# Kernel tuning notes

Measured on AMD Instinct MI355X. Metric: run time of the kernel, lower is better.

Reference implementation:

```python
import jax, jax.numpy as jnp
import numpy as np

N = 20000
E = N * 16
K = 6  # DynamicEdgeConv default k


def feast_conv(x, edge_index, W, u, c, b):
    # PyG FeaStConv with aggr='mean' and added self-loops.
    # q_h = softmax_h(u_h . (x_j - x_i) + c_h); msg = sum_h q_h * (W_h x_j)
    n = x.shape[0]
    heads = u.shape[1]
    out_ch = W.shape[1] // heads
    loops = jnp.arange(n)
    src = jnp.concatenate([edge_index[0], loops])  # x_j (source)
    dst = jnp.concatenate([edge_index[1], loops])  # x_i (target)
    xi = x[dst]
    xj = x[src]
    q = jax.nn.softmax((xj - xi) @ u + c, axis=-1)           # [E+N, H]
    m = (xj @ W).reshape(-1, heads, out_ch)                   # [E+N, H, O]
    msg = (m * q[..., None]).sum(axis=1)                      # [E+N, O]
    agg = jax.ops.segment_sum(msg, dst, num_segments=n)
    cnt = jax.ops.segment_sum(jnp.ones((dst.shape[0],), x.dtype), dst, num_segments=n)
    return agg / jnp.maximum(cnt, 1.0)[:, None] + b


def dynamic_edge_conv(x, W1, b1, W2, b2, k=K):
    # knn_graph (Euclidean, no self-loops) + EdgeConv with max aggregation.
    n = x.shape[0]
    sq = jnp.sum(x * x, axis=1)
    d = sq[:, None] + sq[None, :] - 2.0 * (x @ x.T)           # [N, N] squared dists
    d = d.at[jnp.arange(n), jnp.arange(n)].set(jnp.inf)       # loop=False
    idx = jax.lax.stop_gradient(jax.lax.top_k(-d, k)[1])      # [N, k] neighbors of i
    xj = x[idx]                                               # [N, k, C]
    xi = x[:, None, :]
    tmp = jnp.concatenate([jnp.broadcast_to(xi, xj.shape), xj - xi], axis=-1)
    h = jax.nn.relu(tmp @ W1 + b1) @ W2 + b2                  # mlp on each edge
    return h.max(axis=1)                                      # scatter-max == max over fixed k


def forward(x, edge_index, params):
    (cW1, cu1, cc1, cb1, cW3, cu3, cc3, cb3,
     e1W1, e1b1, e1W2, e1b2, e2W1, e2b1, e2W2, e2b2,
     l1W, l1b, l2W, l2b, l3W, l3b, oW, ob) = params
    x1 = jax.nn.relu(feast_conv(x, edge_index, cW1, cu1, cc1, cb1))      # [N,16]
    y1 = jax.nn.relu(dynamic_edge_conv(x1, e1W1, e1b1, e1W2, e1b2))      # [N,32]
    cat0 = jnp.concatenate([x1, y1], axis=1)                              # [N,48]
    # conv2 output is dead code in the original forward (overwritten), skipped
    y2 = jax.nn.relu(dynamic_edge_conv(y1, e2W1, e2b1, e2W2, e2b2))      # [N,32]
    x3 = jax.nn.relu(feast_conv(cat0, edge_index, cW3, cu3, cc3, cb3))   # [N,64]
    cat1 = jnp.concatenate([x3, y2], axis=1)                              # [N,96]
    h = jax.nn.relu(cat1 @ l1W + l1b)
    h = jax.nn.relu(h @ l2W + l2b)
    h = jax.nn.relu(h @ l3W + l3b)  # double relu in source is idempotent
    return jax.nn.sigmoid(h @ oW + ob)                                    # [N,1]


def setup_inputs() -> dict:
    key = jax.random.key(0)
    ks = jax.random.split(key, 20)
    rn = lambda k, s: jax.random.normal(k, s, jnp.float32) * 0.1
    z = lambda s: jnp.zeros(s, jnp.float32)
    return {
        "x": jax.random.normal(ks[0], (N, 16), jnp.float32),
        "edge_index": jax.random.randint(ks[1], (2, E), 0, N, dtype=jnp.int32),
        # conv1: FeaStConv(16 -> 16, heads=1)
        "cW1": rn(ks[2], (16, 16)), "cu1": rn(ks[3], (16, 1)), "cc1": z((1,)), "cb1": z((16,)),
        # conv3: FeaStConv(48 -> 64, heads=1)
        "cW3": rn(ks[4], (48, 64)), "cu3": rn(ks[5], (48, 1)), "cc3": z((1,)), "cb3": z((64,)),
        # edge1 mlp: Linear(2*16, 32), Linear(32, 32)
        "e1W1": rn(ks[6], (32, 32)), "e1b1": z((32,)), "e1W2": rn(ks[7], (32, 32)), "e1b2": z((32,)),
        # edge2 mlp: Linear(2*32, 32), Linear(32, 32)
        "e2W1": rn(ks[8], (64, 32)), "e2b1": z((32,)), "e2W2": rn(ks[9], (32, 32)), "e2b2": z((32,)),
        # dense head
        "l1W": rn(ks[10], (96, 96)), "l1b": z((96,)),
        "l2W": rn(ks[11], (96, 32)), "l2b": z((32,)),
        "l3W": rn(ks[12], (32, 8)), "l3b": z((8,)),
        "oW": rn(ks[13], (8, 1)), "ob": z((1,)),
    }


def reference(x, edge_index, cW1, cu1, cc1, cb1, cW3, cu3, cc3, cb3,
              e1W1, e1b1, e1W2, e1b2, e2W1, e2b1, e2W2, e2b2,
              l1W, l1b, l2W, l2b, l3W, l3b, oW, ob):
    params = (cW1, cu1, cc1, cb1, cW3, cu3, cc3, cb3,
              e1W1, e1b1, e1W2, e1b2, e2W1, e2b1, e2W2, e2b2,
              l1W, l1b, l2W, l2b, l3W, l3b, oW, ob)
    return forward(x, edge_index, params)
```

## Files before the change

### kernel.cpp

```cpp
#include <hip/hip_runtime.h>
#include <cstdint>

constexpr int Nn = 20000;
constexpr int Ee = 320000;
constexpr int KN = 6;

__global__ __launch_bounds__(256) void scatter16(const float* __restrict__ x,
                                                 const int* __restrict__ ei,
                                                 float* __restrict__ agg,
                                                 int* __restrict__ cnt) {
  int tid = blockIdx.x * 256 + threadIdx.x;
  int e = tid >> 4, c = tid & 15;
  if (e >= Ee) return;
  int s = ei[e], d = ei[Ee + e];
  unsafeAtomicAdd(&agg[d * 16 + c], x[s * 16 + c]);
  if (c == 0) atomicAdd(&cnt[d], 1);
}

__global__ __launch_bounds__(256) void feast1_fin(const float* __restrict__ x,
                                                  const float* __restrict__ agg,
                                                  const int* __restrict__ cnt,
                                                  const float* __restrict__ W,
                                                  const float* __restrict__ b,
                                                  float* __restrict__ x1,
                                                  float* __restrict__ sq) {
  __shared__ float sW[256];
  __shared__ float sb[16];
  sW[threadIdx.x] = W[threadIdx.x];
  if (threadIdx.x < 16) sb[threadIdx.x] = b[threadIdx.x];
  __syncthreads();
  int n = blockIdx.x * 256 + threadIdx.x;
  if (n >= Nn) return;
  float inv = 1.0f / (float)(cnt[n] + 1);
  float v[16];
#pragma unroll
  for (int c = 0; c < 16; ++c) v[c] = (agg[n * 16 + c] + x[n * 16 + c]) * inv;
  float s = 0.0f;
#pragma unroll
  for (int o = 0; o < 16; ++o) {
    float a = sb[o];
#pragma unroll
    for (int c = 0; c < 16; ++c) a = fmaf(v[c], sW[c * 16 + o], a);
    a = fmaxf(a, 0.0f);
    x1[n * 16 + o] = a;
    s = fmaf(a, a, s);
  }
  sq[n] = s;
}

__device__ __forceinline__ void bsins6(float d, int j, float (&bd)[KN], int (&bi)[KN]) {
#pragma unroll
  for (int k = KN - 1; k >= 1; --k) {
    const bool up = d < bd[k - 1];
    const bool at = d < bd[k];
    bd[k] = up ? bd[k - 1] : (at ? d : bd[k]);
    bi[k] = up ? bi[k - 1] : (at ? j : bi[k]);
  }
  const bool at0 = d < bd[0];
  bd[0] = at0 ? d : bd[0];
  bi[0] = at0 ? j : bi[0];
}

template <int C, int U, int TPB>
__global__ __launch_bounds__(TPB, 4) void knn_part(const float* __restrict__ xf,
                                                   const float* __restrict__ sq,
                                                   float* __restrict__ pd,
                                                   int* __restrict__ pi, int chunk) {
  const int row = blockIdx.x * TPB + (int)threadIdx.x;
  const int p = blockIdx.y;
  const int j0 = p * chunk;
  int j1 = j0 + chunk;
  if (j1 > Nn) j1 = Nn;

  float xi[C];
  {
    const float* src = xf + (size_t)(row < Nn ? row : 0) * C;
#pragma unroll
    for (int c = 0; c < C; ++c) xi[c] = src[c];
  }
  float bd[KN];
  int bi[KN];
#pragma unroll
  for (int k = 0; k < KN; ++k) { bd[k] = __builtin_inff(); bi[k] = -1; }

  for (int j = j0; j < j1; j += U) {
    float sv[U];
#pragma unroll
    for (int u = 0; u < U; ++u) {
      const float* xjp = xf + (size_t)(j + u) * C;
      float sqj = sq[j + u];
      float acc = 0.0f;
#pragma unroll
      for (int c = 0; c < C; ++c) acc = fmaf(xi[c], xjp[c], acc);
      float d = fmaf(-2.0f, acc, sqj);
      sv[u] = (j + u == row) ? __builtin_inff() : d;
    }
#pragma unroll
    for (int u = 0; u < U; ++u) bsins6(sv[u], j + u, bd, bi);
  }

  if (row < Nn) {
    size_t base = ((size_t)p * Nn + row) * KN;
    for (int k = 0; k < KN; ++k) { pd[base + k] = bd[k]; pi[base + k] = bi[k]; }
  }
}

__global__ __launch_bounds__(256) void knn_merge(const float* __restrict__ pd,
                                                 const int* __restrict__ pi,
                                                 int* __restrict__ idx, int P) {
  int row = blockIdx.x * 256 + threadIdx.x;
  if (row >= Nn) return;
  float bd[KN];
  int bi[KN];
#pragma unroll
  for (int k = 0; k < KN; ++k) { bd[k] = __builtin_inff(); bi[k] = -1; }
  for (int p = 0; p < P; ++p) {
    size_t base = ((size_t)p * Nn + row) * KN;
#pragma unroll
    for (int k = 0; k < KN; ++k) {
      float d = pd[base + k];
      int id = pi[base + k];
      bsins6(d, id, bd, bi);
    }
  }
  for (int k = 0; k < KN; ++k) idx[row * KN + k] = bi[k];
}

__global__ __launch_bounds__(256) void edge_mlp1(const float* __restrict__ xin,
                                                 const int* __restrict__ idx,
                                                 const float* __restrict__ W1,
                                                 const float* __restrict__ b1,
                                                 const float* __restrict__ W2,
                                                 const float* __restrict__ b2,
                                                 float* __restrict__ yout,
                                                 float* __restrict__ sqout) {
  __shared__ float sW1[1024], sW2[1024], sb1[32], sb2[32];
  __shared__ float xv[8][16], tmp[8][32], hv[8][32];
  int t = threadIdx.x & 31, g = threadIdx.x >> 5;
  for (int i = threadIdx.x; i < 1024; i += 256) { sW1[i] = W1[i]; sW2[i] = W2[i]; }
  if (threadIdx.x < 32) { sb1[threadIdx.x] = b1[threadIdx.x]; sb2[threadIdx.x] = b2[threadIdx.x]; }
  int node = blockIdx.x * 8 + g;
  bool valid = node < Nn;
  int nn = valid ? node : 0;
  if (t < 16) { float v = xin[nn * 16 + t]; xv[g][t] = v; tmp[g][t] = v; }
  __syncthreads();
  float acc = -__builtin_inff();
  for (int k = 0; k < KN; ++k) {
    int j = idx[nn * KN + k];
    if (t < 16) tmp[g][16 + t] = xin[j * 16 + t] - xv[g][t];
    __syncthreads();
    float h = sb1[t];
#pragma unroll
    for (int c = 0; c < 32; ++c) h = fmaf(tmp[g][c], sW1[c * 32 + t], h);
    h = fmaxf(h, 0.0f);
    hv[g][t] = h;
    __syncthreads();
    float o = sb2[t];
#pragma unroll
    for (int c = 0; c < 32; ++c) o = fmaf(hv[g][c], sW2[c * 32 + t], o);
    acc = fmaxf(acc, o);
  }
  float yv = fmaxf(acc, 0.0f);
  if (valid) yout[node * 32 + t] = yv;
  float s = yv * yv;
  s += __shfl_xor(s, 16, 32);
  s += __shfl_xor(s, 8, 32);
  s += __shfl_xor(s, 4, 32);
  s += __shfl_xor(s, 2, 32);
  s += __shfl_xor(s, 1, 32);
  if (valid && t == 0) sqout[node] = s;
}

__global__ __launch_bounds__(256) void edge_mlp2(const float* __restrict__ yin,
                                                 const int* __restrict__ idx,
                                                 const float* __restrict__ W1,
                                                 const float* __restrict__ b1,
                                                 const float* __restrict__ W2,
                                                 const float* __restrict__ b2,
                                                 float* __restrict__ yout) {
  __shared__ float sW1[2048], sW2[1024], sb1[32], sb2[32];
  __shared__ float xv[8][32], tmp[8][64], hv[8][32];
  int t = threadIdx.x & 31, g = threadIdx.x >> 5;
  for (int i = threadIdx.x; i < 2048; i += 256) sW1[i] = W1[i];
  for (int i = threadIdx.x; i < 1024; i += 256) sW2[i] = W2[i];
  if (threadIdx.x < 32) { sb1[threadIdx.x] = b1[threadIdx.x]; sb2[threadIdx.x] = b2[threadIdx.x]; }
  int node = blockIdx.x * 8 + g;
  bool valid = node < Nn;
  int nn = valid ? node : 0;
  { float v = yin[nn * 32 + t]; xv[g][t] = v; tmp[g][t] = v; }
  __syncthreads();
  float acc = -__builtin_inff();
  for (int k = 0; k < KN; ++k) {
    int j = idx[nn * KN + k];
    tmp[g][32 + t] = yin[j * 32 + t] - xv[g][t];
    __syncthreads();
    float h = sb1[t];
#pragma unroll
    for (int c = 0; c < 64; ++c) h = fmaf(tmp[g][c], sW1[c * 32 + t], h);
    h = fmaxf(h, 0.0f);
    hv[g][t] = h;
    __syncthreads();
    float o = sb2[t];
#pragma unroll
    for (int c = 0; c < 32; ++c) o = fmaf(hv[g][c], sW2[c * 32 + t], o);
    acc = fmaxf(acc, o);
  }
  if (valid) yout[node * 32 + t] = fmaxf(acc, 0.0f);
}

__global__ __launch_bounds__(256) void scatter48(const float* __restrict__ x1,
                                                 const float* __restrict__ y1,
                                                 const int* __restrict__ ei,
                                                 float* __restrict__ agg) {
  int tid = blockIdx.x * 256 + threadIdx.x;
  int e = tid / 48, c = tid - e * 48;
  if (e >= Ee) return;
  int s = ei[e], d = ei[Ee + e];
  float v = (c < 16) ? x1[s * 16 + c] : y1[s * 32 + (c - 16)];
  unsafeAtomicAdd(&agg[d * 48 + c], v);
}

__global__ __launch_bounds__(256) void feast3_fin(const float* __restrict__ x1,
                                                  const float* __restrict__ y1,
                                                  const float* __restrict__ agg,
                                                  const int* __restrict__ cnt,
                                                  const float* __restrict__ W,
                                                  const float* __restrict__ b,
                                                  float* __restrict__ x3) {
  __shared__ float sW[3072];
  __shared__ float sb[64];
  for (int i = threadIdx.x; i < 3072; i += 256) sW[i] = W[i];
  if (threadIdx.x < 64) sb[threadIdx.x] = b[threadIdx.x];
  __syncthreads();
  int n = blockIdx.x * 256 + threadIdx.x;
  if (n >= Nn) return;
  float inv = 1.0f / (float)(cnt[n] + 1);
  float v[48];
#pragma unroll
  for (int c = 0; c < 16; ++c) v[c] = (agg[n * 48 + c] + x1[n * 16 + c]) * inv;
#pragma unroll
  for (int c = 16; c < 48; ++c) v[c] = (agg[n * 48 + c] + y1[n * 32 + (c - 16)]) * inv;
  for (int o = 0; o < 64; ++o) {
    float a = sb[o];
#pragma unroll
    for (int c = 0; c < 48; ++c) a = fmaf(v[c], sW[c * 64 + o], a);
    x3[n * 64 + o] = fmaxf(a, 0.0f);
  }
}

__global__ __launch_bounds__(256) void final_mlp(const float* __restrict__ x3,
                                                 const float* __restrict__ y2,
                                                 const float* __restrict__ l1W,
                                                 const float* __restrict__ l1b,
                                                 const float* __restrict__ l2W,
                                                 const float* __restrict__ l2b,
                                                 const float* __restrict__ l3W,
                                                 const float* __restrict__ l3b,
                                                 const float* __restrict__ oW,
                                                 const float* __restrict__ ob,
                                                 float* __restrict__ out) {
  __shared__ float cat[2][96], h1[2][96], h2[2][32], h3[2][8];
  int g = threadIdx.x >> 7, t = threadIdx.x & 127;
  int node = blockIdx.x * 2 + g;
  bool valid = node < Nn;
  int nn = valid ? node : 0;
  if (t < 96) cat[g][t] = (t < 64) ? x3[nn * 64 + t] : y2[nn * 32 + (t - 64)];
  __syncthreads();
  if (t < 96) {
    float a = l1b[t];
#pragma unroll
    for (int c = 0; c < 96; ++c) a = fmaf(cat[g][c], l1W[c * 96 + t], a);
    h1[g][t] = fmaxf(a, 0.0f);
  }
  __syncthreads();
  if (t < 32) {
    float a = l2b[t];
#pragma unroll
    for (int c = 0; c < 96; ++c) a = fmaf(h1[g][c], l2W[c * 32 + t], a);
    h2[g][t] = fmaxf(a, 0.0f);
  }
  __syncthreads();
  if (t < 8) {
    float a = l3b[t];
#pragma unroll
    for (int c = 0; c < 32; ++c) a = fmaf(h2[g][c], l3W[c * 8 + t], a);
    h3[g][t] = fmaxf(a, 0.0f);
  }
  __syncthreads();
  if (t == 0 && valid) {
    float a = ob[0];
#pragma unroll
    for (int c = 0; c < 8; ++c) a = fmaf(h3[g][c], oW[c], a);
    out[node] = 1.0f / (1.0f + expf(-a));
  }
}

extern "C" void kernel_launch(void* const* d_in, const int* in_sizes, int n_in,
                              void* d_out, int out_size, void* d_ws, size_t ws_size,
                              hipStream_t stream) {
  const float* x = (const float*)d_in[0];
  const int* ei = (const int*)d_in[1];
  const float* cW1 = (const float*)d_in[2];
  const float* cb1 = (const float*)d_in[5];
  const float* cW3 = (const float*)d_in[6];
  const float* cb3 = (const float*)d_in[9];
  const float* e1W1 = (const float*)d_in[10];
  const float* e1b1 = (const float*)d_in[11];
  const float* e1W2 = (const float*)d_in[12];
  const float* e1b2 = (const float*)d_in[13];
  const float* e2W1 = (const float*)d_in[14];
  const float* e2b1 = (const float*)d_in[15];
  const float* e2W2 = (const float*)d_in[16];
  const float* e2b2 = (const float*)d_in[17];
  const float* l1W = (const float*)d_in[18];
  const float* l1b = (const float*)d_in[19];
  const float* l2W = (const float*)d_in[20];
  const float* l2b = (const float*)d_in[21];
  const float* l3W = (const float*)d_in[22];
  const float* l3b = (const float*)d_in[23];
  const float* oW = (const float*)d_in[24];
  const float* ob = (const float*)d_in[25];
  float* out = (float*)d_out;

  char* p = (char*)d_ws;
  auto alloc = [&](size_t bytes) {
    char* r = p;
    p += (bytes + 255) & ~(size_t)255;
    return r;
  };
  float* x1 = (float*)alloc((size_t)Nn * 16 * 4);
  float* y1 = (float*)alloc((size_t)Nn * 32 * 4);
  float* y2 = (float*)alloc((size_t)Nn * 32 * 4);
  float* x3 = (float*)alloc((size_t)Nn * 64 * 4);
  float* agg = (float*)alloc((size_t)Nn * 48 * 4);
  int* cnt = (int*)alloc((size_t)Nn * 4);
  float* sqb = (float*)alloc((size_t)Nn * 4);
  int* idx1 = (int*)alloc((size_t)Nn * KN * 4);
  int* idx2 = (int*)alloc((size_t)Nn * KN * 4);
  size_t fixed_bytes = (size_t)(p - (char*)d_ws);
  size_t per_chunk = (size_t)Nn * KN * 4 * 2 + 512;
  int P = 16;
  if (fixed_bytes + (size_t)P * per_chunk > ws_size) {
    size_t avail = ws_size > fixed_bytes ? ws_size - fixed_bytes : 0;
    int pmax = (int)(avail / per_chunk);
    P = pmax < 1 ? 1 : pmax;
    if (P > 16) P = 16;
  }
  float* pd = (float*)alloc((size_t)P * Nn * KN * 4);
  int* pi = (int*)alloc((size_t)P * Nn * KN * 4);
  int chunk = (((Nn + P - 1) / P) + 3) & ~3;

  hipMemsetAsync(agg, 0, (size_t)Nn * 16 * 4, stream);
  hipMemsetAsync(cnt, 0, (size_t)Nn * 4, stream);
  scatter16<<<(Ee * 16) / 256, 256, 0, stream>>>(x, ei, agg, cnt);
  feast1_fin<<<(Nn + 255) / 256, 256, 0, stream>>>(x, agg, cnt, cW1, cb1, x1, sqb);

  {
    dim3 grid((Nn + 255) / 256, P);
    knn_part<16, 4, 256><<<grid, 256, 0, stream>>>(x1, sqb, pd, pi, chunk);
    knn_merge<<<(Nn + 255) / 256, 256, 0, stream>>>(pd, pi, idx1, P);
  }

  edge_mlp1<<<(Nn + 7) / 8, 256, 0, stream>>>(x1, idx1, e1W1, e1b1, e1W2, e1b2, y1, sqb);

  {
    dim3 grid((Nn + 255) / 256, P);
    knn_part<32, 2, 256><<<grid, 256, 0, stream>>>(y1, sqb, pd, pi, chunk);
    knn_merge<<<(Nn + 255) / 256, 256, 0, stream>>>(pd, pi, idx2, P);
  }

  edge_mlp2<<<(Nn + 7) / 8, 256, 0, stream>>>(y1, idx2, e2W1, e2b1, e2W2, e2b2, y2);

  hipMemsetAsync(agg, 0, (size_t)Nn * 48 * 4, stream);
  scatter48<<<(Ee * 48) / 256, 256, 0, stream>>>(x1, y1, ei, agg);
  feast3_fin<<<(Nn + 255) / 256, 256, 0, stream>>>(x1, y1, agg, cnt, cW3, cb3, x3);

  final_mlp<<<(Nn + 1) / 2, 256, 0, stream>>>(x3, y2, l1W, l1b, l2W, l2b, l3W, l3b,
                                              oW, ob, out);
}
```

Baseline: 1.685 ms.

## Split kNN into value-only pass, threshold, and filtered index pass

The kNN search now makes two passes. The first keeps only the 6 smallest distances per row, using a cheap min/max network with no index tracking, and a merge kernel turns these into a per-row 6th-nearest threshold. A second pass recomputes all distances and runs the full index-tracking insertion only for candidates at or below that threshold, so most insertion work is skipped. The cost is computing the full distance matrix twice and launching two extra kernels, and the launch-bounds occupancy hint is dropped.

```diff
diff --git a/kernel.cpp b/kernel.cpp
--- a/kernel.cpp
+++ b/kernel.cpp
@@ -48,6 +48,12 @@
   sq[n] = s;
 }
 
+__device__ __forceinline__ void bsv6(float d, float (&bd)[KN]) {
+#pragma unroll
+  for (int k = KN - 1; k >= 1; --k) bd[k] = fminf(fmaxf(bd[k - 1], d), bd[k]);
+  bd[0] = fminf(bd[0], d);
+}
+
 __device__ __forceinline__ void bsins6(float d, int j, float (&bd)[KN], int (&bi)[KN]) {
 #pragma unroll
   for (int k = KN - 1; k >= 1; --k) {
@@ -62,10 +68,9 @@
 }
 
 template <int C, int U, int TPB>
-__global__ __launch_bounds__(TPB, 4) void knn_part(const float* __restrict__ xf,
-                                                   const float* __restrict__ sq,
-                                                   float* __restrict__ pd,
-                                                   int* __restrict__ pi, int chunk) {
+__global__ __launch_bounds__(TPB) void knn_val(const float* __restrict__ xf,
+                                               const float* __restrict__ sq,
+                                               float* __restrict__ pv, int chunk) {
   const int row = blockIdx.x * TPB + (int)threadIdx.x;
   const int p = blockIdx.y;
   const int j0 = p * chunk;
@@ -79,12 +84,10 @@
     for (int c = 0; c < C; ++c) xi[c] = src[c];
   }
   float bd[KN];
-  int bi[KN];
-#pragma unroll
-  for (int k = 0; k < KN; ++k) { bd[k] = __builtin_inff(); bi[k] = -1; }
+#pragma unroll
+  for (int k = 0; k < KN; ++k) bd[k] = __builtin_inff();
 
   for (int j = j0; j < j1; j += U) {
-    float sv[U];
 #pragma unroll
     for (int u = 0; u < U; ++u) {
       const float* xjp = xf + (size_t)(j + u) * C;
@@ -93,10 +96,78 @@
 #pragma unroll
       for (int c = 0; c < C; ++c) acc = fmaf(xi[c], xjp[c], acc);
       float d = fmaf(-2.0f, acc, sqj);
+      d = (j + u == row) ? __builtin_inff() : d;
+      bsv6(d, bd);
+    }
+  }
+
+  if (row < Nn) {
+    size_t base = ((size_t)p * Nn + row) * KN;
+#pragma unroll
+    for (int k = 0; k < KN; ++k) pv[base + k] = bd[k];
+  }
+}
+
+__global__ __launch_bounds__(256) void knn_thr(const float* __restrict__ pv,
+                                               float* __restrict__ thr, int P) {
+  int row = blockIdx.x * 256 + threadIdx.x;
+  if (row >= Nn) return;
+  float bd[KN];
+#pragma unroll
+  for (int k = 0; k < KN; ++k) bd[k] = __builtin_inff();
+  for (int p = 0; p < P; ++p) {
+    size_t base = ((size_t)p * Nn + row) * KN;
+#pragma unroll
+    for (int k = 0; k < KN; ++k) bsv6(pv[base + k], bd);
+  }
+  thr[row] = bd[5];
+}
+
+template <int C, int U, int TPB>
+__global__ __launch_bounds__(TPB) void knn_hit(const float* __restrict__ xf,
+                                               const float* __restrict__ sq,
+                                               const float* __restrict__ thr,
+                                               float* __restrict__ pd,
+                                               int* __restrict__ pi, int chunk) {
+  const int row = blockIdx.x * TPB + (int)threadIdx.x;
+  const int p = blockIdx.y;
+  const int j0 = p * chunk;
+  int j1 = j0 + chunk;
+  if (j1 > Nn) j1 = Nn;
+
+  const int rc = row < Nn ? row : 0;
+  float xi[C];
+  {
+    const float* src = xf + (size_t)rc * C;
+#pragma unroll
+    for (int c = 0; c < C; ++c) xi[c] = src[c];
+  }
+  const float thrv = thr[rc];
+  float bd[KN];
+  int bi[KN];
+#pragma unroll
+  for (int k = 0; k < KN; ++k) { bd[k] = __builtin_inff(); bi[k] = -1; }
+
+  for (int j = j0; j < j1; j += U) {
+    float sv[U];
+#pragma unroll
+    for (int u = 0; u < U; ++u) {
+      const float* xjp = xf + (size_t)(j + u) * C;
+      float sqj = sq[j + u];
+      float acc = 0.0f;
+#pragma unroll
+      for (int c = 0; c < C; ++c) acc = fmaf(xi[c], xjp[c], acc);
+      float d = fmaf(-2.0f, acc, sqj);
       sv[u] = (j + u == row) ? __builtin_inff() : d;
     }
-#pragma unroll
-    for (int u = 0; u < U; ++u) bsins6(sv[u], j + u, bd, bi);
+    float mn = sv[0];
+#pragma unroll
+    for (int u = 1; u < U; ++u) mn = fminf(mn, sv[u]);
+    if (mn <= thrv) {
+#pragma unroll
+      for (int u = 0; u < U; ++u)
+        if (sv[u] <= thrv) bsins6(sv[u], j + u, bd, bi);
+    }
   }
 
   if (row < Nn) {
@@ -118,9 +189,7 @@
     size_t base = ((size_t)p * Nn + row) * KN;
 #pragma unroll
     for (int k = 0; k < KN; ++k) {
-      float d = pd[base + k];
-      int id = pi[base + k];
-      bsins6(d, id, bd, bi);
+      bsins6(pd[base + k], pi[base + k], bd, bi);
     }
   }
   for (int k = 0; k < KN; ++k) idx[row * KN + k] = bi[k];
@@ -335,6 +404,7 @@
   float* agg = (float*)alloc((size_t)Nn * 48 * 4);
   int* cnt = (int*)alloc((size_t)Nn * 4);
   float* sqb = (float*)alloc((size_t)Nn * 4);
+  float* thr = (float*)alloc((size_t)Nn * 4);
   int* idx1 = (int*)alloc((size_t)Nn * KN * 4);
   int* idx2 = (int*)alloc((size_t)Nn * KN * 4);
   size_t fixed_bytes = (size_t)(p - (char*)d_ws);
@@ -349,31 +419,36 @@
   float* pd = (float*)alloc((size_t)P * Nn * KN * 4);
   int* pi = (int*)alloc((size_t)P * Nn * KN * 4);
   int chunk = (((Nn + P - 1) / P) + 3) & ~3;
+  const int gx = (Nn + 255) / 256;
 
   hipMemsetAsync(agg, 0, (size_t)Nn * 16 * 4, stream);
   hipMemsetAsync(cnt, 0, (size_t)Nn * 4, stream);
   scatter16<<<(Ee * 16) / 256, 256, 0, stream>>>(x, ei, agg, cnt);
-  feast1_fin<<<(Nn + 255) / 256, 256, 0, stream>>>(x, agg, cnt, cW1, cb1, x1, sqb);
+  feast1_fin<<<gx, 256, 0, stream>>>(x, agg, cnt, cW1, cb1, x1, sqb);
 
   {
-    dim3 grid((Nn + 255) / 256, P);
-    knn_part<16, 4, 256><<<grid, 256, 0, stream>>>(x1, sqb, pd, pi, chunk);
-    knn_merge<<<(Nn + 255) / 256, 256, 0, stream>>>(pd, pi, idx1, P);
+    dim3 grid(gx, P);
+    knn_val<16, 4, 256><<<grid, 256, 0, stream>>>(x1, sqb, pd, chunk);
+    knn_thr<<<gx, 256, 0, stream>>>(pd, thr, P);
+    knn_hit<16, 4, 256><<<grid, 256, 0, stream>>>(x1, sqb, thr, pd, pi, chunk);
+    knn_merge<<<gx, 256, 0, stream>>>(pd, pi, idx1, P);
   }
 
   edge_mlp1<<<(Nn + 7) / 8, 256, 0, stream>>>(x1, idx1, e1W1, e1b1, e1W2, e1b2, y1, sqb);
 
   {
-    dim3 grid((Nn + 255) / 256, P);
-    knn_part<32, 2, 256><<<grid, 256, 0, stream>>>(y1, sqb, pd, pi, chunk);
-    knn_merge<<<(Nn + 255) / 256, 256, 0, stream>>>(pd, pi, idx2, P);
+    dim3 grid(gx, P);
+    knn_val<32, 2, 256><<<grid, 256, 0, stream>>>(y1, sqb, pd, chunk);
+    knn_thr<<<gx, 256, 0, stream>>>(pd, thr, P);
+    knn_hit<32, 2, 256><<<grid, 256, 0, stream>>>(y1, sqb, thr, pd, pi, chunk);
+    knn_merge<<<gx, 256, 0, stream>>>(pd, pi, idx2, P);
   }
 
   edge_mlp2<<<(Nn + 7) / 8, 256, 0, stream>>>(y1, idx2, e2W1, e2b1, e2W2, e2b2, y2);
 
   hipMemsetAsync(agg, 0, (size_t)Nn * 48 * 4, stream);
   scatter48<<<(Ee * 48) / 256, 256, 0, stream>>>(x1, y1, ei, agg);
-  feast3_fin<<<(Nn + 255) / 256, 256, 0, stream>>>(x1, y1, agg, cnt, cW3, cb3, x3);
+  feast3_fin<<<gx, 256, 0, stream>>>(x1, y1, agg, cnt, cW3, cb3, x3);
 
   final_mlp<<<(Nn + 1) / 2, 256, 0, stream>>>(x3, y2, l1W, l1b, l2W, l2b, l3W, l3b,
                                               oW, ob, out);
```

After: 2.046 ms. 21.4% more time.
